# Optimization experiments

Hardware: AMD Instinct MI355X
Metric: run time of the kernel (lower is better)

## Reference

```python
import jax, jax.numpy as jnp
import numpy as np

B, T, D_MODEL = 2, 2048, 1024
H, D_HEAD, R = 16, 64, 16
CAUSAL = True


def setup_inputs() -> dict:
    key = jax.random.key(0)
    ks = jax.random.split(key, 6)
    return {
        "x": jax.random.normal(ks[0], (B, T, D_MODEL), dtype=jnp.float32),
        "W_qkv": jax.random.normal(ks[1], (D_MODEL, 3 * D_MODEL), dtype=jnp.float32) * 0.02,
        "W_q_lsr": jax.random.normal(ks[2], (H, D_HEAD, R), dtype=jnp.float32) * 0.1,
        "W_k_lsr": jax.random.normal(ks[3], (H, D_HEAD, R), dtype=jnp.float32) * 0.1,
        "core": jax.random.normal(ks[4], (H, R), dtype=jnp.float32),
        "W_o": jax.random.normal(ks[5], (D_MODEL, D_MODEL), dtype=jnp.float32) * 0.02,
    }


def reference(x, W_qkv, W_q_lsr, W_k_lsr, core, W_o):
    Bx, Tx, D = x.shape
    Hh, Dh, Rr = W_q_lsr.shape
    # Fused QKV projection, then split heads -> (B, H, T, D_head)
    qkv = x @ W_qkv  # (B, T, 3D)
    q, k, v = jnp.split(qkv, 3, axis=-1)
    q = q.reshape(Bx, Tx, Hh, Dh).transpose(0, 2, 1, 3)
    k = k.reshape(Bx, Tx, Hh, Dh).transpose(0, 2, 1, 3)
    v = v.reshape(Bx, Tx, Hh, Dh).transpose(0, 2, 1, 3)
    # Low-rank (LSR) projections of q and k; core + 1/sqrt(R) scaling on q side
    scale = 1.0 / jnp.sqrt(jnp.asarray(max(Rr, 1), dtype=jnp.float32))
    q_lr = jnp.einsum('bhtd,hdr->bhtr', q, W_q_lsr) * core[None, :, None, :] * scale
    k_lr = jnp.einsum('bhtd,hdr->bhtr', k, W_k_lsr)
    # Low-rank scores (B, H, T, T)
    scores = jnp.einsum('bhir,bhjr->bhij', q_lr, k_lr)
    if CAUSAL:
        mask = jnp.tril(jnp.ones((Tx, Tx), dtype=bool))
        scores = jnp.where(mask[None, None], scores, -jnp.inf)
    attn = jax.nn.softmax(scores, axis=-1)
    out = jnp.einsum('bhij,bhjd->bhid', attn, v)  # (B, H, T, D_head)
    out = out.transpose(0, 2, 1, 3).reshape(Bx, Tx, D)
    return out @ W_o
```

## Files before the change

### kernel.cpp

```cpp
#include <hip/hip_runtime.h>
#include <hip/hip_bf16.h>

#define BB 2
#define TT 2048
#define DD 1024
#define HH 16
#define DH 64
#define RR 16
#define BT (BB*TT)
#define BH (BB*HH)
#define D3 (3*DD)
#define NC 1536

typedef __bf16 bf16x8 __attribute__((ext_vector_type(8)));
typedef __bf16 bf16x4 __attribute__((ext_vector_type(4)));
typedef float f32x4 __attribute__((ext_vector_type(4)));
typedef short short4v __attribute__((ext_vector_type(4)));

__device__ __forceinline__ float bf2f(unsigned short u) {
  unsigned int v = ((unsigned int)u) << 16;
  return __builtin_bit_cast(float, v);
}
__device__ __forceinline__ unsigned short f2bf(float f) {
  unsigned int x = __builtin_bit_cast(unsigned int, f);
  unsigned int r = x + 0x7fffu + ((x >> 16) & 1u);
  return (unsigned short)(r >> 16);
}
__device__ __forceinline__ short4v pack_bf16x4(float a, float b, float c, float d) {
  uint2 u;
  u.x = (unsigned)f2bf(a) | ((unsigned)f2bf(b) << 16);
  u.y = (unsigned)f2bf(c) | ((unsigned)f2bf(d) << 16);
  return __builtin_bit_cast(short4v, u);
}
__device__ __forceinline__ short4v pack4_cvt(float a, float b, float c, float d) {
  bf16x4 v = {(__bf16)a, (__bf16)b, (__bf16)c, (__bf16)d};
  return __builtin_bit_cast(short4v, v);
}

#define NEG_BIG (-1e30f)

__device__ __forceinline__ void async_copy16(const void* g, void* l) {
  __builtin_amdgcn_global_load_lds((const __attribute__((address_space(1))) void*)g,
                                   (__attribute__((address_space(3))) void*)l, 16, 0, 0);
}

__global__ __launch_bounds__(256) void prep_fused(const float* __restrict__ x,
                                                  const float* __restrict__ Wqkv,
                                                  const float* __restrict__ Wql,
                                                  const float* __restrict__ Wkl,
                                                  const float* __restrict__ core,
                                                  const float* __restrict__ Wo,
                                                  unsigned short* __restrict__ x_bf,
                                                  unsigned short* __restrict__ Wcomb_t,
                                                  unsigned short* __restrict__ Wo_t) {
  __shared__ float tile[32][33];
  __shared__ float Aq[64][65], Ak[64][65], Lq[64][16], Lk[64][16], cs[16];
  const int bid = blockIdx.x, tid = threadIdx.x;
  if (bid < 2048) {
    int i = (bid * 256 + tid) * 8;
    float4 a = *(const float4*)&x[i];
    float4 b = *(const float4*)&x[i + 4];
    unsigned short t[8] = {f2bf(a.x), f2bf(a.y), f2bf(a.z), f2bf(a.w),
                           f2bf(b.x), f2bf(b.y), f2bf(b.z), f2bf(b.w)};
    *(uint4*)&x_bf[i] = *(const uint4*)t;
  } else if (bid < 4096) {
    const float* in; unsigned short* out; int C, coff, lb;
    if (bid < 3072) { in = Wo;   out = Wo_t;    C = DD; coff = 0;    lb = bid - 2048; }
    else            { in = Wqkv; out = Wcomb_t; C = D3; coff = 2048; lb = bid - 3072; }
    const int tx = tid & 31, ty = tid >> 5;
    const int bx = lb & 31, by = lb >> 5;
    const int xx = bx * 32 + tx, y0 = by * 32;
#pragma unroll
    for (int i = 0; i < 32; i += 8)
      tile[ty + i][tx] = in[(size_t)(y0 + ty + i) * C + coff + xx];
    __syncthreads();
    const int xo = y0 + tx, yo0 = bx * 32;
#pragma unroll
    for (int i = 0; i < 32; i += 8)
      out[(size_t)(yo0 + ty + i) * DD + xo] = f2bf(tile[tx][ty + i]);
  } else {
    const int l = bid - 4096;
    const int d0 = (l & 15) * 64, h = l >> 4;
#pragma unroll
    for (int p = 0; p < 16; p++) {
      int idx = p * 256 + tid, dd = idx >> 6, e = idx & 63;
      Aq[dd][e] = Wqkv[(size_t)(d0 + dd) * D3 + h * 64 + e];
      Ak[dd][e] = Wqkv[(size_t)(d0 + dd) * D3 + DD + h * 64 + e];
    }
#pragma unroll
    for (int p = 0; p < 4; p++) {
      int idx = p * 256 + tid, e = idx >> 4, r = idx & 15;
      Lq[e][r] = Wql[h * 1024 + e * 16 + r];
      Lk[e][r] = Wkl[h * 1024 + e * 16 + r];
    }
    if (tid < 16) cs[tid] = core[h * 16 + tid];
    __syncthreads();
    const int dd = tid & 63, rg = tid >> 6;
    float aq[4] = {}, ak[4] = {};
    for (int e = 0; e < 64; e++) {
      float xq = Aq[dd][e], xk = Ak[dd][e];
#pragma unroll
      for (int j = 0; j < 4; j++) {
        aq[j] += xq * Lq[e][rg * 4 + j];
        ak[j] += xk * Lk[e][rg * 4 + j];
      }
    }
#pragma unroll
    for (int j = 0; j < 4; j++) {
      int r = rg * 4 + j;
      Wcomb_t[(size_t)(1024 + h * 16 + r) * DD + d0 + dd] =
          f2bf(aq[j] * cs[r] * (0.25f * 1.4426950408889634f));
      Wcomb_t[(size_t)(1280 + h * 16 + r) * DD + d0 + dd] = f2bf(ak[j]);
    }
  }
}

__device__ __forceinline__ void gemm64_core(const unsigned short* __restrict__ A,
                                            const unsigned short* __restrict__ Bt,
                                            int K, int bm, int bn,
                                            int tid, int g, int c, int wm, int wn,
                                            f32x4 acc[2][4]) {
  __shared__ __attribute__((aligned(16))) unsigned short As[2][2 * 2048];
  __shared__ __attribute__((aligned(16))) unsigned short Bs[2][2 * 4096];
  const int e0 = tid * 8;
  const int r0 = e0 >> 5, q0 = e0 & 31;
  const unsigned short* Ar  = &A[(size_t)(bm * 64 + r0) * K + q0];
  const unsigned short* Br0 = &Bt[(size_t)(bn * 128 + r0) * K + q0];
  const unsigned short* Br1 = &Bt[(size_t)(bn * 128 + 64 + r0) * K + q0];
  async_copy16(Ar,       &As[0][e0]);
  async_copy16(Ar  + 32, &As[0][2048 + e0]);
  async_copy16(Br0,      &Bs[0][e0]);
  async_copy16(Br1,      &Bs[0][2048 + e0]);
  async_copy16(Br0 + 32, &Bs[0][4096 + e0]);
  async_copy16(Br1 + 32, &Bs[0][4096 + 2048 + e0]);
  __syncthreads();
  const int nsteps = K >> 6;
  for (int t = 0; t < nsteps; t++) {
    const int cur = t & 1, nxt = cur ^ 1;
    if (t + 1 < nsteps) {
      const int k1 = (t + 1) << 6;
      async_copy16(Ar  + k1,      &As[nxt][e0]);
      async_copy16(Ar  + k1 + 32, &As[nxt][2048 + e0]);
      async_copy16(Br0 + k1,      &Bs[nxt][e0]);
      async_copy16(Br1 + k1,      &Bs[nxt][2048 + e0]);
      async_copy16(Br0 + k1 + 32, &Bs[nxt][4096 + e0]);
      async_copy16(Br1 + k1 + 32, &Bs[nxt][4096 + 2048 + e0]);
    }
#pragma unroll
    for (int p = 0; p < 2; p++) {
      bf16x8 af[2];
#pragma unroll
      for (int mt = 0; mt < 2; mt++)
        af[mt] = *(const bf16x8*)&As[cur][p * 2048 + (wm * 32 + mt * 16 + c) * 32 + g * 8];
#pragma unroll
      for (int nt = 0; nt < 4; nt++) {
        bf16x8 bf = *(const bf16x8*)&Bs[cur][p * 4096 + (wn * 64 + nt * 16 + c) * 32 + g * 8];
#pragma unroll
        for (int mt = 0; mt < 2; mt++)
          acc[mt][nt] = __builtin_amdgcn_mfma_f32_16x16x32_bf16(af[mt], bf, acc[mt][nt], 0, 0, 0);
      }
    }
    __syncthreads();
  }
}

__global__ __launch_bounds__(256) void gemm64_f32(const unsigned short* __restrict__ A,
                                                  const unsigned short* __restrict__ Bt,
                                                  float* __restrict__ C,
                                                  int M, int N, int K) {
  const int tid = threadIdx.x, lane = tid & 63;
  const int g = lane >> 4, c = lane & 15;
  const int wid = tid >> 6, wm = wid >> 1, wn = wid & 1;
  const int bm = blockIdx.y, bn = blockIdx.x;
  f32x4 acc[2][4] = {};
  gemm64_core(A, Bt, K, bm, bn, tid, g, c, wm, wn, acc);
#pragma unroll
  for (int mt = 0; mt < 2; mt++)
#pragma unroll
    for (int nt = 0; nt < 4; nt++)
#pragma unroll
      for (int r = 0; r < 4; r++) {
        int row = bm * 64 + wm * 32 + mt * 16 + g * 4 + r;
        int col = bn * 128 + wn * 64 + nt * 16 + c;
        C[(size_t)row * N + col] = acc[mt][nt][r];
      }
}

__global__ __launch_bounds__(256) void gemm_fused(const unsigned short* __restrict__ A,
                                                  const unsigned short* __restrict__ Bt,
                                                  unsigned short* __restrict__ qls,
                                                  unsigned short* __restrict__ klr,
                                                  unsigned short* __restrict__ vt,
                                                  int M, int N, int K) {
  const int tid = threadIdx.x, lane = tid & 63;
  const int g = lane >> 4, c = lane & 15;
  const int wid = tid >> 6, wm = wid >> 1, wn = wid & 1;
  const int bm = blockIdx.y, bn = blockIdx.x;
  f32x4 acc[2][4] = {};
  gemm64_core(A, Bt, K, bm, bn, tid, g, c, wm, wn, acc);
#pragma unroll
  for (int mt = 0; mt < 2; mt++)
#pragma unroll
    for (int nt = 0; nt < 4; nt++) {
      int colb = bn * 128 + wn * 64 + nt * 16;
      int tg0 = bm * 64 + wm * 32 + mt * 16 + g * 4;
      int b = tg0 >> 11, t0 = tg0 & 2047;
      if (colb < 1024) {
        int h = colb >> 6, d = (colb & 63) + c;
        uint2 pk = __builtin_bit_cast(uint2, pack_bf16x4(acc[mt][nt][0], acc[mt][nt][1],
                                                         acc[mt][nt][2], acc[mt][nt][3]));
        size_t idx = (size_t)(b * 16 + h) * (TT / 4) * 256 + (size_t)(t0 >> 2) * 256 + d * 4;
        *(uint2*)&vt[idx] = pk;
      } else if (colb < 1280) {
        int h = (colb - 1024) >> 4;
        size_t base = (size_t)(b * 16 + h) * TT;
#pragma unroll
        for (int r = 0; r < 4; r++)
          qls[(base + t0 + r) * 16 + c] = f2bf(acc[mt][nt][r]);
      } else {
        int h = (colb - 1280) >> 4;
        size_t base = (size_t)(b * 16 + h) * TT;
#pragma unroll
        for (int r = 0; r < 4; r++)
          klr[(base + t0 + r) * 16 + c] = f2bf(acc[mt][nt][r]);
      }
    }
}

__global__ __launch_bounds__(256, 2) void flash_lsr(const unsigned short* __restrict__ qls,
                                                    const unsigned short* __restrict__ klr,
                                                    const unsigned short* __restrict__ vt,
                                                    unsigned short* __restrict__ attn) {
  const int bh = blockIdx.x & 31, b = bh >> 4, h = bh & 15;
  const int i = blockIdx.x >> 5;
  const int qt = (i < 8) ? (15 - i) : (i - 8);
  const int tid = threadIdx.x, lane = tid & 63, w = tid >> 6;
  const int g = lane >> 4, c = lane & 15;
  const int q0 = qt * 128, jmax = qt;

  __shared__ __attribute__((aligned(16))) unsigned short Ks[2][128 * 20];

  const size_t qbase = (size_t)bh * TT;
  const short4v qfA = __builtin_bit_cast(short4v,
      *(const uint2*)&qls[(qbase + q0 + w * 16 + c) * 16 + g * 4]);
  const short4v qfB = __builtin_bit_cast(short4v,
      *(const uint2*)&qls[(qbase + q0 + 64 + w * 16 + c) * 16 + g * 4]);
  const int qgA = q0 + w * 16 + c, qgB = qgA + 64;
  float miA = NEG_BIG, liA = 0.f, miB = NEG_BIG, liB = 0.f;
  f32x4 oaA[4] = {}, oaB[4] = {};
  const f32x4 zero = {0.f, 0.f, 0.f, 0.f};
  const size_t kb = (size_t)bh * TT * 16;
  const size_t vb = (size_t)bh * TT * 64;

  uint4 kr = *(const uint4*)&klr[kb + tid * 8];

  int p = 0;
  f32x4 sA[8], sB[8];
  for (int jt = 0; jt <= jmax; jt++) {
    *(uint4*)&Ks[p][(tid >> 1) * 20 + (tid & 1) * 8] = kr;
    __syncthreads();
    if (jt < jmax)
      kr = *(const uint4*)&klr[kb + (size_t)(jt + 1) * 2048 + tid * 8];
    const unsigned short* Kb = Ks[p];
#pragma unroll
    for (int nt = 0; nt < 8; nt++) {
      short4v kf = __builtin_bit_cast(short4v, *(const uint2*)&Kb[(nt * 16 + c) * 20 + g * 4]);
      sA[nt] = __builtin_amdgcn_mfma_f32_16x16x16bf16_1k(kf, qfA, zero, 0, 0, 0);
      sB[nt] = __builtin_amdgcn_mfma_f32_16x16x16bf16_1k(kf, qfB, zero, 0, 0, 0);
    }
    if (jt == jmax) {
#pragma unroll
      for (int nt = 0; nt < 8; nt++)
#pragma unroll
        for (int r = 0; r < 4; r++) {
          int jg = jt * 128 + nt * 16 + g * 4 + r;
          if (jg > qgA) sA[nt][r] = NEG_BIG;
          if (jg > qgB) sB[nt][r] = NEG_BIG;
        }
    }
    auto softmax = [&](f32x4 (&s)[8], float& mi, float& li, f32x4 (&oa)[4]) {
      f32x4 vm = s[0];
#pragma unroll
      for (int nt = 1; nt < 8; nt++)
#pragma unroll
        for (int r = 0; r < 4; r++) vm[r] = fmaxf(vm[r], s[nt][r]);
      float rm = fmaxf(fmaxf(vm[0], vm[1]), fmaxf(vm[2], vm[3]));
      rm = fmaxf(rm, __shfl_xor(rm, 16, 64));
      rm = fmaxf(rm, __shfl_xor(rm, 32, 64));
      float mnew = fmaxf(mi, rm);
      float alpha = __builtin_amdgcn_exp2f(mi - mnew);
      mi = mnew;
      f32x4 vs = zero;
#pragma unroll
      for (int nt = 0; nt < 8; nt++)
#pragma unroll
        for (int r = 0; r < 4; r++) {
          float pv = __builtin_amdgcn_exp2f(s[nt][r] - mnew);
          s[nt][r] = pv;
          vs[r] += pv;
        }
      float rs = (vs[0] + vs[1]) + (vs[2] + vs[3]);
      rs += __shfl_xor(rs, 16, 64);
      rs += __shfl_xor(rs, 32, 64);
      li = li * alpha + rs;
#pragma unroll
      for (int nd = 0; nd < 4; nd++)
#pragma unroll
        for (int r = 0; r < 4; r++) oa[nd][r] *= alpha;
    };
    softmax(sA, miA, liA, oaA);
    softmax(sB, miB, liB, oaB);
    const unsigned short* vp = &vt[vb + (size_t)jt * 8192];
#pragma unroll
    for (int kc = 0; kc < 8; kc++) {
      short4v pfA = pack4_cvt(sA[kc][0], sA[kc][1], sA[kc][2], sA[kc][3]);
      short4v pfB = pack4_cvt(sB[kc][0], sB[kc][1], sB[kc][2], sB[kc][3]);
#pragma unroll
      for (int nd = 0; nd < 4; nd++) {
        uint2 vv = *(const uint2*)&vp[(kc * 4 + g) * 256 + (nd * 16 + c) * 4];
        short4v vf = __builtin_bit_cast(short4v, vv);
        oaA[nd] = __builtin_amdgcn_mfma_f32_16x16x16bf16_1k(vf, pfA, oaA[nd], 0, 0, 0);
        oaB[nd] = __builtin_amdgcn_mfma_f32_16x16x16bf16_1k(vf, pfB, oaB[nd], 0, 0, 0);
      }
    }
    p ^= 1;
  }

  const float invA = 1.f / liA, invB = 1.f / liB;
  const size_t rowA = ((size_t)b * TT + q0 + w * 16 + c) * DD + h * 64;
  const size_t rowB = rowA + (size_t)64 * DD;
#pragma unroll
  for (int nd = 0; nd < 4; nd++) {
    short4v pkA = pack4_cvt(oaA[nd][0] * invA, oaA[nd][1] * invA,
                            oaA[nd][2] * invA, oaA[nd][3] * invA);
    *(uint2*)&attn[rowA + nd * 16 + g * 4] = __builtin_bit_cast(uint2, pkA);
    short4v pkB = pack4_cvt(oaB[nd][0] * invB, oaB[nd][1] * invB,
                            oaB[nd][2] * invB, oaB[nd][3] * invB);
    *(uint2*)&attn[rowB + nd * 16 + g * 4] = __builtin_bit_cast(uint2, pkB);
  }
}

extern "C" void kernel_launch(void* const* d_in, const int* in_sizes, int n_in,
                              void* d_out, int out_size, void* d_ws, size_t ws_size,
                              hipStream_t stream) {
  const float* x      = (const float*)d_in[0];
  const float* W_qkv  = (const float*)d_in[1];
  const float* W_qlsr = (const float*)d_in[2];
  const float* W_klsr = (const float*)d_in[3];
  const float* core   = (const float*)d_in[4];
  const float* W_o    = (const float*)d_in[5];
  float* out = (float*)d_out;

  char* ws = (char*)d_ws;
  unsigned short* x_bf    = (unsigned short*)ws; ws += (size_t)BT * DD * 2;
  unsigned short* Wcomb_t = (unsigned short*)ws; ws += (size_t)NC * DD * 2;
  unsigned short* Wo_t    = (unsigned short*)ws; ws += (size_t)DD * DD * 2;
  unsigned short* qls     = (unsigned short*)ws; ws += (size_t)BH * TT * 16 * 2;
  unsigned short* klr     = (unsigned short*)ws; ws += (size_t)BH * TT * 16 * 2;
  unsigned short* vt      = (unsigned short*)ws; ws += (size_t)BH * TT * 64 * 2;
  unsigned short* attn    = (unsigned short*)ws; ws += (size_t)BT * DD * 2;

  prep_fused<<<4352, 256, 0, stream>>>(x, W_qkv, W_qlsr, W_klsr, core, W_o,
                                       x_bf, Wcomb_t, Wo_t);
  gemm_fused<<<dim3(NC / 128, BT / 64), 256, 0, stream>>>(x_bf, Wcomb_t, qls, klr, vt, BT, NC, DD);
  flash_lsr<<<dim3(16 * BH), 256, 0, stream>>>(qls, klr, vt, attn);
  gemm64_f32<<<dim3(DD / 128, BT / 64), 256, 0, stream>>>(attn, Wo_t, out, BT, DD, DD);
}
```

Measured before the change: 167.3 us.

## Deepen GEMM pipeline to 4-stage ring with K=32 steps and explicit waitcnt

Replaces the double-buffered K=64 shared-memory pipeline with a 4-buffer ring of K=32 stages that keeps three stages of async copies in flight. Explicit s_waitcnt vmcnt counts and raw s_barrier replace __syncthreads, so the loop waits only for the stage about to be consumed. The aim is to hide global-load latency better in the projection GEMMs. In exchange there are more barriers per K element and a more fragile hand-counted wait scheme.

```diff
diff --git a/kernel.cpp b/kernel.cpp
--- a/kernel.cpp
+++ b/kernel.cpp
@@ -120,47 +120,46 @@
                                             int K, int bm, int bn,
                                             int tid, int g, int c, int wm, int wn,
                                             f32x4 acc[2][4]) {
-  __shared__ __attribute__((aligned(16))) unsigned short As[2][2 * 2048];
-  __shared__ __attribute__((aligned(16))) unsigned short Bs[2][2 * 4096];
+  __shared__ __attribute__((aligned(16))) unsigned short As[4][2048];
+  __shared__ __attribute__((aligned(16))) unsigned short Bs[4][4096];
   const int e0 = tid * 8;
   const int r0 = e0 >> 5, q0 = e0 & 31;
   const unsigned short* Ar  = &A[(size_t)(bm * 64 + r0) * K + q0];
   const unsigned short* Br0 = &Bt[(size_t)(bn * 128 + r0) * K + q0];
   const unsigned short* Br1 = &Bt[(size_t)(bn * 128 + 64 + r0) * K + q0];
-  async_copy16(Ar,       &As[0][e0]);
-  async_copy16(Ar  + 32, &As[0][2048 + e0]);
-  async_copy16(Br0,      &Bs[0][e0]);
-  async_copy16(Br1,      &Bs[0][2048 + e0]);
-  async_copy16(Br0 + 32, &Bs[0][4096 + e0]);
-  async_copy16(Br1 + 32, &Bs[0][4096 + 2048 + e0]);
-  __syncthreads();
-  const int nsteps = K >> 6;
+  auto stage = [&](int s) {
+    const int b = s & 3, k = s << 5;
+    async_copy16(Ar  + k, &As[b][e0]);
+    async_copy16(Br0 + k, &Bs[b][e0]);
+    async_copy16(Br1 + k, &Bs[b][2048 + e0]);
+  };
+  stage(0); stage(1); stage(2);
+  asm volatile("s_waitcnt vmcnt(6)" ::: "memory");
+  __builtin_amdgcn_s_barrier();
+  __builtin_amdgcn_sched_barrier(0);
+  const int nsteps = K >> 5;
   for (int t = 0; t < nsteps; t++) {
-    const int cur = t & 1, nxt = cur ^ 1;
+    const int cur = t & 3;
+    const bool pf = (t + 3 < nsteps);
+    if (pf) stage(t + 3);
+    bf16x8 af[2];
+#pragma unroll
+    for (int mt = 0; mt < 2; mt++)
+      af[mt] = *(const bf16x8*)&As[cur][(wm * 32 + mt * 16 + c) * 32 + g * 8];
+#pragma unroll
+    for (int nt = 0; nt < 4; nt++) {
+      bf16x8 bf = *(const bf16x8*)&Bs[cur][(wn * 64 + nt * 16 + c) * 32 + g * 8];
+#pragma unroll
+      for (int mt = 0; mt < 2; mt++)
+        acc[mt][nt] = __builtin_amdgcn_mfma_f32_16x16x32_bf16(af[mt], bf, acc[mt][nt], 0, 0, 0);
+    }
     if (t + 1 < nsteps) {
-      const int k1 = (t + 1) << 6;
-      async_copy16(Ar  + k1,      &As[nxt][e0]);
-      async_copy16(Ar  + k1 + 32, &As[nxt][2048 + e0]);
-      async_copy16(Br0 + k1,      &Bs[nxt][e0]);
-      async_copy16(Br1 + k1,      &Bs[nxt][2048 + e0]);
-      async_copy16(Br0 + k1 + 32, &Bs[nxt][4096 + e0]);
-      async_copy16(Br1 + k1 + 32, &Bs[nxt][4096 + 2048 + e0]);
-    }
-#pragma unroll
-    for (int p = 0; p < 2; p++) {
-      bf16x8 af[2];
-#pragma unroll
-      for (int mt = 0; mt < 2; mt++)
-        af[mt] = *(const bf16x8*)&As[cur][p * 2048 + (wm * 32 + mt * 16 + c) * 32 + g * 8];
-#pragma unroll
-      for (int nt = 0; nt < 4; nt++) {
-        bf16x8 bf = *(const bf16x8*)&Bs[cur][p * 4096 + (wn * 64 + nt * 16 + c) * 32 + g * 8];
-#pragma unroll
-        for (int mt = 0; mt < 2; mt++)
-          acc[mt][nt] = __builtin_amdgcn_mfma_f32_16x16x32_bf16(af[mt], bf, acc[mt][nt], 0, 0, 0);
-      }
-    }
-    __syncthreads();
+      if (pf)                    asm volatile("s_waitcnt vmcnt(6) lgkmcnt(0)" ::: "memory");
+      else if (t + 2 < nsteps)   asm volatile("s_waitcnt vmcnt(3) lgkmcnt(0)" ::: "memory");
+      else                       asm volatile("s_waitcnt vmcnt(0) lgkmcnt(0)" ::: "memory");
+      __builtin_amdgcn_s_barrier();
+      __builtin_amdgcn_sched_barrier(0);
+    }
   }
 }
 
```

New measurement: 176.2 us. +5.3%, slower.
